# Kernel tuning notes

Hardware: AMD Instinct MI355X
Metric: run time of the kernel (lower is better)

The kernel has to match this reference:

```python
import jax, jax.numpy as jnp
import numpy as np

B, N_PTS, M_ROIS = 2, 8192, 2048
C_IN, O, H, NS = 128, 256, 4, 32
RADIUS = 1.6
BN_EPS = 1e-5
SCALE = 10.0  # point cloud extent


def setup_inputs() -> dict:
    key = jax.random.key(0)
    ks = jax.random.split(key, 20)
    f32 = jnp.float32
    Cg = C_IN + 3  # grouper concats relative xyz to features

    def kaiming(k, shape, fan_in):
        return jax.random.normal(k, shape, f32) * np.sqrt(2.0 / fan_in)

    inp = {
        "xyz": jax.random.uniform(ks[0], (B, N_PTS, 3), f32) * SCALE,
        "new_xyz": jax.random.uniform(ks[1], (B, M_ROIS, 3), f32) * SCALE,
        "features": jax.random.normal(ks[2], (B, C_IN, N_PTS), f32),
        # conv1d (kernel=1, no bias) weights, torch layout (out, in)
        "pos_w": kaiming(ks[3], (O, 3), 3),
        "key_w": kaiming(ks[4], (O, Cg), Cg),
        "val_w1": kaiming(ks[5], (O, Cg), Cg),
        "bn1_g": jnp.ones((O,), f32), "bn1_b": jnp.zeros((O,), f32),
        "val_w2": kaiming(ks[6], (O, O), O),
        "bn2_g": jnp.ones((O,), f32), "bn2_b": jnp.zeros((O,), f32),
        "attn_w": kaiming(ks[7], (H, O), O),
        # sigmoid-gated coefficient linears (no bias)
        "kc_w": kaiming(ks[8], (O, O), O),
        "qc_w": kaiming(ks[9], (O, O), O),
        "qkc_w": kaiming(ks[10], (O, O), O),
        "vc_w": kaiming(ks[11], (O, O), O),
        # cls/reg weight MLPs: Linear(O,O//2)+ReLU, Linear(O//2,1)+Sigmoid
        "cls_w1": kaiming(ks[12], (O // 2, O), O), "cls_b1": jnp.zeros((O // 2,), f32),
        "cls_w2": kaiming(ks[13], (1, O // 2), O // 2), "cls_b2": jnp.zeros((1,), f32),
        "reg_w1": kaiming(ks[14], (O // 2, O), O), "reg_b1": jnp.zeros((O // 2,), f32),
        "reg_w2": kaiming(ks[15], (1, O // 2), O // 2), "reg_b2": jnp.zeros((1,), f32),
    }
    return inp


def _bn(x, g, b):
    # eval-mode BatchNorm1d with running_mean=0, running_var=1 (init state)
    return g[None, :, None] * (x * (1.0 / np.sqrt(1.0 + BN_EPS))) + b[None, :, None]


def _conv1x1(w, x):  # (O,C) x (M,C,NS) -> (M,O,NS)
    return jnp.einsum('oc,mcn->mon', w, x)


def _ball_group(pts, q):
    # ball query: first NS points within RADIUS of each query (pad with first hit)
    n_tot = pts.shape[0]
    d2 = jnp.sum((q[:, None, :] - pts[None, :, :]) ** 2, axis=-1)  # (M, Ntot)
    order = jnp.where(d2 < RADIUS ** 2, jnp.arange(n_tot, dtype=jnp.int32), n_tot)
    neg_vals, idx = jax.lax.top_k(-order, NS)  # smallest indices among in-ball pts
    valid = (-neg_vals) < n_tot
    idx = jnp.where(valid, idx, idx[:, :1])  # pad with first neighbor
    has_any = valid[:, :1]
    idx = jnp.where(has_any, idx, 0)  # empty balls -> point 0
    return idx, ~has_any[:, 0]


def reference(xyz, new_xyz, features, pos_w, key_w, val_w1, bn1_g, bn1_b,
              val_w2, bn2_g, bn2_b, attn_w, kc_w, qc_w, qkc_w, vc_w,
              cls_w1, cls_b1, cls_w2, cls_b2, reg_w1, reg_b1, reg_w2, reg_b2):
    pts = xyz.reshape(-1, 3)                                   # (Ntot, 3)
    feats = features.transpose(0, 2, 1).reshape(-1, C_IN)      # (Ntot, C)
    q = new_xyz.reshape(-1, 3)                                 # (M, 3)

    idx, empty_mask = _ball_group(pts, q)                      # (M, NS)
    gx = pts[idx] - q[:, None, :]                              # relative xyz (M,NS,3)
    gxt = gx.transpose(0, 2, 1)                                # (M,3,NS)
    gf = jnp.concatenate([gx, feats[idx]], axis=-1).transpose(0, 2, 1)  # (M,C+3,NS)

    pos = jax.nn.relu(_conv1x1(pos_w, gxt))                    # (M,O,NS)
    key = jax.nn.relu(_conv1x1(key_w, gf))                     # (M,O,NS)
    v = jax.nn.relu(_bn(_conv1x1(val_w1, gf), bn1_g, bn1_b))
    val = jax.nn.relu(_bn(_conv1x1(val_w2, v), bn2_g, bn2_b))  # (M,O,NS)
    pos_key = pos * key

    sig = jax.nn.sigmoid
    v_c = sig(pos.mean(2) @ vc_w.T)                            # (M,O)
    q_c = sig(pos.mean(2) @ qc_w.T)
    k_c = sig(key.mean(2) @ kc_w.T)
    qk_c = sig(pos_key.mean(2) @ qkc_w.T)

    val = val + pos * v_c[:, :, None]
    attn_emb = pos * q_c[:, :, None] + key * k_c[:, :, None] + pos_key * qk_c[:, :, None]
    attn = jax.nn.softmax(jnp.einsum('ho,mon->mhn', attn_w, attn_emb), axis=-1)  # (M,H,NS)

    m = val.shape[0]
    vh = val.reshape(m, H, O // H, NS)
    new_features = jnp.einsum('mhdn,mhn->mhd', vh, attn).reshape(m, O)  # (M,O)

    def gate(x, w1, b1, w2, b2):
        return sig(jax.nn.relu(x @ w1.T + b1) @ w2.T + b2)

    cls_features = new_features * gate(new_features, cls_w1, cls_b1, cls_w2, cls_b2)
    reg_features = new_features * gate(new_features, reg_w1, reg_b1, reg_w2, reg_b2)
    return new_features, cls_features, reg_features
```

## Files before the change

kernel.cpp:

```cpp
#include <hip/hip_runtime.h>

#define DI __device__ __forceinline__

typedef __attribute__((ext_vector_type(8))) short bf16x8;
typedef __attribute__((ext_vector_type(4))) short s16x4;
typedef __attribute__((ext_vector_type(4))) float f32x4;

DI short f2bs(float x){ unsigned u = __float_as_uint(x);
  return (short)((u + 0x7FFF + ((u >> 16) & 1)) >> 16); }
DI float bs2f(short s){ return __uint_as_float(((unsigned)(unsigned short)s) << 16); }
DI f32x4 MFMA(bf16x8 a, bf16x8 b, f32x4 c){
  return __builtin_amdgcn_mfma_f32_16x16x32_bf16(a, b, c, 0, 0, 0);
}

constexpr int NP   = 8192;
constexpr int NTOT = 16384;
constexpr int M    = 4096;
constexpr int C    = 128;
constexpr int O    = 256;
constexpr int NS   = 32;
constexpr int H    = 4;
constexpr int KP   = 160;
constexpr int GFS  = 168;
constexpr int VS   = 264;
constexpr float BNS = 0.99999500003749969f;

DI void copy_rows(short* __restrict__ dst, const short* __restrict__ src, int t){
  int row = t >> 3, s = (t & 7) * 8;
  const short* sp = src + row*VS + s;
  short* dp = dst + (size_t)row*O + s;
  #pragma unroll
  for(int j = 0; j < 4; j++)
    *(bf16x8*)(dp + j*64) = *(const bf16x8*)(sp + j*64);
}

__global__ __launch_bounds__(256) void k_transpose(const float* __restrict__ feat,
                                                   short* __restrict__ fT){
  __shared__ float tile[128][65];
  int blk = blockIdx.x;
  int b  = blk >> 7;
  int n0 = (blk & 127) << 6;
  int t = threadIdx.x;
  int nn = t & 63, c4 = t >> 6;
  const float* src = feat + (size_t)b * C * NP;
  for(int i = 0; i < 32; i++){
    int c = c4 * 32 + i;
    tile[c][nn] = src[(size_t)c * NP + n0 + nn];
  }
  __syncthreads();
  int c2 = t & 127, nb = t >> 7;
  for(int j = 0; j < 32; j++){
    int n = nb + j * 2;
    fT[((size_t)(b * NP + n0 + n)) * C + c2] = f2bs(tile[c2][n]);
  }
}

__global__ __launch_bounds__(256) void k_pack(
    const float* __restrict__ kw, const float* __restrict__ v1w,
    const float* __restrict__ v2w,
    const float* __restrict__ vcw, const float* __restrict__ qcw,
    const float* __restrict__ kcw, const float* __restrict__ qkcw,
    const float* __restrict__ cw1, const float* __restrict__ rw1,
    short* __restrict__ keyP, short* __restrict__ v1P,
    short* __restrict__ v2b,
    short* __restrict__ gw,
    short* __restrict__ cw1b, short* __restrict__ rw1b)
{
  int i = blockIdx.x * 256 + threadIdx.x;
  if(i < O * KP){
    int o = i / KP, k = i % KP;
    float a = 0.0f, b = 0.0f;
    if(k < 128){ a = kw[o*131 + 3 + k]; b = v1w[o*131 + 3 + k]; }
    else if(k < 131){ a = kw[o*131 + (k - 128)]; b = v1w[o*131 + (k - 128)]; }
    keyP[i] = f2bs(a);
    v1P[i]  = f2bs(b);
  }
  if(i < O * O){
    v2b[i] = f2bs(v2w[i]);
    gw[0*O*O + i] = f2bs(vcw[i]);
    gw[1*O*O + i] = f2bs(qcw[i]);
    gw[2*O*O + i] = f2bs(kcw[i]);
    gw[3*O*O + i] = f2bs(qkcw[i]);
  }
  if(i < (O/2) * O){
    cw1b[i] = f2bs(cw1[i]);
    rw1b[i] = f2bs(rw1[i]);
  }
}

__global__ __launch_bounds__(64) void k_ballq(const float* __restrict__ xyz,
                                              const float* __restrict__ nxyz,
                                              int* __restrict__ idxo,
                                              float* __restrict__ gxo){
#pragma clang fp contract(off)
  int m = blockIdx.x;
  int lane = threadIdx.x;
  float qx = nxyz[m*3+0], qy = nxyz[m*3+1], qz = nxyz[m*3+2];
  __shared__ int sel[NS];
  int cnt = 0;
  for(int base = 0; base < NTOT; base += 64){
    int p = base + lane;
    float dx = qx - xyz[p*3+0], dy = qy - xyz[p*3+1], dz = qz - xyz[p*3+2];
    float d2 = dx*dx + dy*dy;
    d2 = d2 + dz*dz;
    bool pred = d2 < 2.56f;
    unsigned long long bal = __ballot(pred);
    if(pred){
      int pos = cnt + __popcll(bal & ((1ull << lane) - 1ull));
      if(pos < NS) sel[pos] = p;
    }
    cnt += __popcll(bal);
    if(cnt >= NS) break;
  }
  __syncthreads();
  if(lane < NS){
    int s = 0;
    if(cnt > 0) s = (lane < cnt) ? sel[lane] : sel[0];
    idxo[m*NS + lane] = s;
    gxo[(m*NS+lane)*3+0] = xyz[s*3+0] - qx;
    gxo[(m*NS+lane)*3+1] = xyz[s*3+1] - qy;
    gxo[(m*NS+lane)*3+2] = xyz[s*3+2] - qz;
  }
}

__global__ __launch_bounds__(256, 5) void k_conv(
    const short* __restrict__ fT,
    const short* __restrict__ keyP, const short* __restrict__ v1P,
    const short* __restrict__ v2b,
    const float* __restrict__ posw,
    const float* __restrict__ g1, const float* __restrict__ b1,
    const float* __restrict__ g2, const float* __restrict__ b2,
    const int* __restrict__ idxw, const float* __restrict__ gxw,
    short* __restrict__ keyo, short* __restrict__ valo,
    float* __restrict__ mPos, float* __restrict__ mKey, float* __restrict__ mPK,
    int q0)
{
  int lq = blockIdx.x, q = q0 + lq, t = threadIdx.x;
  int w = t >> 6, l = t & 63;
  int col = l & 15, kq = l >> 4;
  int ro = w * 64;
  __shared__ __align__(16) short gf[NS * GFS];
  __shared__ __align__(16) short vbuf[NS * VS];
  __shared__ float gxs[NS * 4];
  __shared__ int  sel[NS];
  if(t < NS){
    sel[t] = idxw[q*NS + t];
    gxs[t*4+0] = gxw[(q*NS+t)*3+0];
    gxs[t*4+1] = gxw[(q*NS+t)*3+1];
    gxs[t*4+2] = gxw[(q*NS+t)*3+2];
    gxs[t*4+3] = 0.0f;
  }
  __syncthreads();
  for(int i = 0; i < 8; i++){
    int n = w*8 + i;
    int p = sel[n];
    *(unsigned*)&gf[n*GFS + l*2] = *(const unsigned*)(fT + (size_t)p * C + l*2);
  }
  {
    int n = t & 31, kk = (t >> 5) * 4;
    for(int j = 0; j < 4; j++){
      int k = kk + j;
      float v = (k < 3) ? gxs[n*4 + k] : 0.0f;
      gf[n*GFS + 128 + k] = f2bs(v);
    }
  }
  __syncthreads();

  float posR[4][2][4];
  for(int mt=0;mt<4;mt++) for(int r=0;r<4;r++){
    int o = ro + mt*16 + kq*4 + r;
    float w0 = posw[o*3+0], w1 = posw[o*3+1], w2 = posw[o*3+2];
    for(int nt=0;nt<2;nt++){
      int n = nt*16 + col;
      posR[mt][nt][r] = fmaxf(w0*gxs[n*4+0] + w1*gxs[n*4+1] + w2*gxs[n*4+2], 0.0f);
    }
  }

  f32x4 acc[4][2];
  const f32x4 vzero = {0.0f, 0.0f, 0.0f, 0.0f};

  for(int mt=0;mt<4;mt++) for(int nt=0;nt<2;nt++) acc[mt][nt] = vzero;
  for(int ks = 0; ks < 5; ks++){
    bf16x8 b0 = *(const bf16x8*)&gf[col*GFS + ks*32 + kq*8];
    bf16x8 b1v = *(const bf16x8*)&gf[(16+col)*GFS + ks*32 + kq*8];
    for(int mt = 0; mt < 4; mt++){
      bf16x8 a = *(const bf16x8*)(keyP + (size_t)(ro + mt*16 + col)*KP + ks*32 + kq*8);
      acc[mt][0] = MFMA(a, b0, acc[mt][0]);
      acc[mt][1] = MFMA(a, b1v, acc[mt][1]);
    }
  }
  float mS[4][4][3];
  for(int mt=0;mt<4;mt++){
    for(int nt=0;nt<2;nt++){
      s16x4 pk;
      for(int r=0;r<4;r++){
        float v = fmaxf(acc[mt][nt][r], 0.0f);
        pk[r] = f2bs(v);
        if(nt == 0){ mS[mt][r][0] = posR[mt][0][r];  mS[mt][r][1] = v;
                     mS[mt][r][2] = posR[mt][0][r]*v; }
        else       { mS[mt][r][0] += posR[mt][1][r]; mS[mt][r][1] += v;
                     mS[mt][r][2] += posR[mt][1][r]*v; }
      }
      int n = nt*16 + col;
      *(s16x4*)&vbuf[n*VS + ro + mt*16 + kq*4] = pk;
    }
  }
  __syncthreads();
  copy_rows(keyo + (size_t)lq*NS*O, vbuf, t);
  for(int mt=0;mt<4;mt++) for(int r=0;r<4;r++){
    float sp = mS[mt][r][0], sk = mS[mt][r][1], spk = mS[mt][r][2];
    for(int msk=1; msk<16; msk<<=1){
      sp += __shfl_xor(sp, msk); sk += __shfl_xor(sk, msk); spk += __shfl_xor(spk, msk);
    }
    if(col == 0){
      int o = ro + mt*16 + kq*4 + r;
      mPos[lq*O+o] = sp  * 0.03125f;
      mKey[lq*O+o] = sk  * 0.03125f;
      mPK [lq*O+o] = spk * 0.03125f;
    }
  }

  for(int mt=0;mt<4;mt++) for(int nt=0;nt<2;nt++) acc[mt][nt] = vzero;
  for(int ks = 0; ks < 5; ks++){
    bf16x8 b0 = *(const bf16x8*)&gf[col*GFS + ks*32 + kq*8];
    bf16x8 b1v = *(const bf16x8*)&gf[(16+col)*GFS + ks*32 + kq*8];
    for(int mt = 0; mt < 4; mt++){
      bf16x8 a = *(const bf16x8*)(v1P + (size_t)(ro + mt*16 + col)*KP + ks*32 + kq*8);
      acc[mt][0] = MFMA(a, b0, acc[mt][0]);
      acc[mt][1] = MFMA(a, b1v, acc[mt][1]);
    }
  }
  __syncthreads();
  for(int mt=0;mt<4;mt++){
    int o0 = ro + mt*16 + kq*4;
    float gg[4], bb[4];
    for(int r=0;r<4;r++){ gg[r] = g1[o0+r]; bb[r] = b1[o0+r]; }
    for(int nt=0;nt<2;nt++){
      s16x4 pk;
      for(int r=0;r<4;r++)
        pk[r] = f2bs(fmaxf(gg[r]*(acc[mt][nt][r] * BNS) + bb[r], 0.0f));
      int n = nt*16 + col;
      *(s16x4*)&vbuf[n*VS + o0] = pk;
    }
  }
  __syncthreads();

  for(int mt=0;mt<4;mt++) for(int nt=0;nt<2;nt++) acc[mt][nt] = vzero;
  for(int ks = 0; ks < 8; ks++){
    bf16x8 b0 = *(const bf16x8*)&vbuf[col*VS + ks*32 + kq*8];
    bf16x8 b1v = *(const bf16x8*)&vbuf[(16+col)*VS + ks*32 + kq*8];
    for(int mt = 0; mt < 4; mt++){
      bf16x8 a = *(const bf16x8*)(v2b + (size_t)(ro + mt*16 + col)*O + ks*32 + kq*8);
      acc[mt][0] = MFMA(a, b0, acc[mt][0]);
      acc[mt][1] = MFMA(a, b1v, acc[mt][1]);
    }
  }
  s16x4 valS[4][2];
  for(int mt=0;mt<4;mt++){
    int o0 = ro + mt*16 + kq*4;
    float gg[4], bb[4];
    for(int r=0;r<4;r++){ gg[r] = g2[o0+r]; bb[r] = b2[o0+r]; }
    for(int nt=0;nt<2;nt++)
      for(int r=0;r<4;r++)
        valS[mt][nt][r] = f2bs(fmaxf(gg[r]*(acc[mt][nt][r] * BNS) + bb[r], 0.0f));
  }
  __syncthreads();
  for(int mt=0;mt<4;mt++) for(int nt=0;nt<2;nt++){
    int n = nt*16 + col;
    *(s16x4*)&vbuf[n*VS + ro + mt*16 + kq*4] = valS[mt][nt];
  }
  __syncthreads();
  copy_rows(valo + (size_t)lq*NS*O, vbuf, t);
}

__global__ __launch_bounds__(256) void k_gates(
    const float* __restrict__ mPos, const float* __restrict__ mKey,
    const float* __restrict__ mPK, const short* __restrict__ gw,
    float* __restrict__ gates)
{
  int t = threadIdx.x, w = t >> 6, l = t & 63, col = l & 15, kq = l >> 4;
  int lq0 = blockIdx.x * 16;
  const float* A  = (w < 2) ? mPos : ((w == 2) ? mKey : mPK);
  const short* Wg = gw + (size_t)w * O * O;
  f32x4 acc[16];
  const f32x4 vzero = {0.0f,0.0f,0.0f,0.0f};
  for(int i=0;i<16;i++) acc[i] = vzero;
  for(int ks = 0; ks < 8; ks++){
    union { bf16x8 v; short e[8]; } u;
    const float* ap = A + (size_t)(lq0 + col)*O + ks*32 + kq*8;
    for(int j = 0; j < 8; j++) u.e[j] = f2bs(ap[j]);
    for(int nt = 0; nt < 16; nt++){
      bf16x8 bv = *(const bf16x8*)(Wg + (size_t)(nt*16 + col)*O + ks*32 + kq*8);
      acc[nt] = MFMA(u.v, bv, acc[nt]);
    }
  }
  for(int nt=0;nt<16;nt++) for(int r=0;r<4;r++){
    int lqq = lq0 + kq*4 + r;
    int oo = nt*16 + col;
    gates[((size_t)lqq*4 + w)*O + oo] = 1.0f / (1.0f + expf(-acc[nt][r]));
  }
}

__global__ __launch_bounds__(256) void k_attn(
    const short* __restrict__ keyw, const short* __restrict__ valw,
    const float* __restrict__ gxw, const float* __restrict__ posw,
    const float* __restrict__ attw, const float* __restrict__ gates,
    float* __restrict__ outNF, int q0)
{
  int lq = blockIdx.x, q = q0 + lq, t = threadIdx.x;
  __shared__ float emL[O * 33];
  __shared__ float attnL[H * NS];
  __shared__ float gxs[NS * 3];
  __shared__ float partial[256];
  if(t < 96) gxs[t] = gxw[q*96 + t];
  float vc  = gates[((size_t)lq*4 + 0)*O + t];
  float qc  = gates[((size_t)lq*4 + 1)*O + t];
  float kc  = gates[((size_t)lq*4 + 2)*O + t];
  float qkc = gates[((size_t)lq*4 + 3)*O + t];
  float pw0 = posw[t*3+0], pw1 = posw[t*3+1], pw2 = posw[t*3+2];
  __syncthreads();
  float posr[NS];
  for(int n = 0; n < NS; n++)
    posr[n] = fmaxf(pw0*gxs[n*3] + pw1*gxs[n*3+1] + pw2*gxs[n*3+2], 0.0f);
  for(int n = 0; n < NS; n++){
    float k = bs2f(keyw[((size_t)lq*NS + n)*O + t]);
    emL[t*33 + n] = posr[n]*qc + k*kc + posr[n]*k*qkc;
  }
  __syncthreads();
  {
    int idx = t & 127, h = idx >> 5, n = idx & 31, half = t >> 7;
    float s = 0;
    const float* aw = attw + h*O + half*128;
    for(int o = 0; o < 128; o++) s += aw[o] * emL[(half*128 + o)*33 + n];
    partial[t] = s;
  }
  __syncthreads();
  if(t < 128){
    int h = t >> 5, n = t & 31;
    float s = partial[t] + partial[t + 128];
    float mx = s;
    for(int msk=1; msk<32; msk<<=1) mx = fmaxf(mx, __shfl_xor(mx, msk));
    float e = expf(s - mx);
    float sum = e;
    for(int msk=1; msk<32; msk<<=1) sum += __shfl_xor(sum, msk);
    attnL[h*NS + n] = e / sum;
  }
  __syncthreads();
  int h = t >> 6;
  float nf = 0;
  for(int n = 0; n < NS; n++){
    float v = bs2f(valw[((size_t)lq*NS + n)*O + t]);
    nf += (v + posr[n]*vc) * attnL[h*NS + n];
  }
  outNF[(size_t)q*O + t] = nf;
}

__global__ __launch_bounds__(256) void k_fgate(
    const float* __restrict__ nf,
    const short* __restrict__ cw1b, const float* __restrict__ cb1,
    const float* __restrict__ cw2, const float* __restrict__ cb2,
    const short* __restrict__ rw1b, const float* __restrict__ rb1,
    const float* __restrict__ rw2, const float* __restrict__ rb2,
    float* __restrict__ outC, float* __restrict__ outR)
{
  int t = threadIdx.x, w = t >> 6, l = t & 63, col = l & 15, kq = l >> 4;
  int q0 = blockIdx.x * 64;
  __shared__ float sC[64], sR[64];
  f32x4 acc[16];
  const f32x4 vzero = {0.0f,0.0f,0.0f,0.0f};
  for(int i=0;i<16;i++) acc[i] = vzero;
  int arow = q0 + w*16 + col;
  for(int ks = 0; ks < 8; ks++){
    union { bf16x8 v; short e[8]; } u;
    const float* ap = nf + (size_t)arow*O + ks*32 + kq*8;
    for(int j = 0; j < 8; j++) u.e[j] = f2bs(ap[j]);
    for(int nt = 0; nt < 16; nt++){
      const short* W1 = (nt < 8) ? cw1b : rw1b;
      int j = (nt & 7)*16 + col;
      bf16x8 bv = *(const bf16x8*)(W1 + (size_t)j*O + ks*32 + kq*8);
      acc[nt] = MFMA(u.v, bv, acc[nt]);
    }
  }
  for(int r = 0; r < 4; r++){
    float pc = 0, pr = 0;
    for(int nt = 0; nt < 8; nt++){
      int j = nt*16 + col;
      pc += fmaxf(acc[nt][r] + cb1[j], 0.0f) * cw2[j];
    }
    for(int nt = 8; nt < 16; nt++){
      int j = (nt - 8)*16 + col;
      pr += fmaxf(acc[nt][r] + rb1[j], 0.0f) * rw2[j];
    }
    for(int msk=1; msk<16; msk<<=1){ pc += __shfl_xor(pc, msk); pr += __shfl_xor(pr, msk); }
    if(col == 0){
      int qq = w*16 + kq*4 + r;
      sC[qq] = 1.0f / (1.0f + expf(-(pc + cb2[0])));
      sR[qq] = 1.0f / (1.0f + expf(-(pr + rb2[0])));
    }
  }
  __syncthreads();
  for(int qq = 0; qq < 64; qq++){
    float nv = nf[(size_t)(q0 + qq)*O + t];
    outC[(size_t)(q0 + qq)*O + t] = nv * sC[qq];
    outR[(size_t)(q0 + qq)*O + t] = nv * sR[qq];
  }
}

extern "C" void kernel_launch(void* const* d_in, const int* in_sizes, int n_in,
                              void* d_out, int out_size, void* d_ws, size_t ws_size,
                              hipStream_t stream)
{
  const float* xyz  = (const float*)d_in[0];
  const float* nxyz = (const float*)d_in[1];
  const float* feat = (const float*)d_in[2];
  const float* posw = (const float*)d_in[3];
  const float* keyw = (const float*)d_in[4];
  const float* v1w  = (const float*)d_in[5];
  const float* bn1g = (const float*)d_in[6];
  const float* bn1b = (const float*)d_in[7];
  const float* v2w  = (const float*)d_in[8];
  const float* bn2g = (const float*)d_in[9];
  const float* bn2b = (const float*)d_in[10];
  const float* attw = (const float*)d_in[11];
  const float* kcw  = (const float*)d_in[12];
  const float* qcw  = (const float*)d_in[13];
  const float* qkcw = (const float*)d_in[14];
  const float* vcw  = (const float*)d_in[15];
  const float* cw1  = (const float*)d_in[16];
  const float* cb1  = (const float*)d_in[17];
  const float* cw2  = (const float*)d_in[18];
  const float* cb2  = (const float*)d_in[19];
  const float* rw1  = (const float*)d_in[20];
  const float* rb1  = (const float*)d_in[21];
  const float* rw2  = (const float*)d_in[22];
  const float* rb2  = (const float*)d_in[23];

  const size_t fixedB = 12000000;
  const size_t perQ   = 40960;
  int Q = 64;
  for(int cand : {4096, 2048, 1024, 512, 256, 128}){
    if(fixedB + (size_t)cand*perQ <= ws_size){ Q = cand; break; }
  }

  char* p = (char*)d_ws;
  auto alloc = [&](size_t bytes){ char* r = p; p += (bytes + 255) & ~size_t(255); return r; };
  short* fT    = (short*)alloc((size_t)NTOT*C*2);
  short* keyP  = (short*)alloc((size_t)O*KP*2);
  short* v1P   = (short*)alloc((size_t)O*KP*2);
  short* v2b   = (short*)alloc((size_t)O*O*2);
  short* gw    = (short*)alloc((size_t)4*O*O*2);
  short* cw1b  = (short*)alloc((size_t)(O/2)*O*2);
  short* rw1b  = (short*)alloc((size_t)(O/2)*O*2);
  int*   idxw  = (int*)  alloc((size_t)M*NS*4);
  float* gxw   = (float*)alloc((size_t)M*NS*3*4);
  short* keyo  = (short*)alloc((size_t)Q*NS*O*2);
  short* valo  = (short*)alloc((size_t)Q*NS*O*2);
  float* mPos  = (float*)alloc((size_t)Q*O*4);
  float* mKey  = (float*)alloc((size_t)Q*O*4);
  float* mPK   = (float*)alloc((size_t)Q*O*4);
  float* gates = (float*)alloc((size_t)Q*4*O*4);

  float* outNF = (float*)d_out;
  float* outC  = outNF + (size_t)M*O;
  float* outR  = outC  + (size_t)M*O;

  k_transpose<<<256, 256, 0, stream>>>(feat, fT);
  k_pack     <<<256, 256, 0, stream>>>(keyw, v1w, v2w, vcw, qcw, kcw, qkcw, cw1, rw1,
                                       keyP, v1P, v2b, gw, cw1b, rw1b);
  k_ballq    <<<M,   64,  0, stream>>>(xyz, nxyz, idxw, gxw);
  for(int q0 = 0; q0 < M; q0 += Q){
    k_conv  <<<Q,    256, 0, stream>>>(fT, keyP, v1P, v2b,
                                       posw, bn1g, bn1b, bn2g, bn2b,
                                       idxw, gxw, keyo, valo, mPos, mKey, mPK, q0);
    k_gates <<<Q/16, 256, 0, stream>>>(mPos, mKey, mPK, gw, gates);
    k_attn  <<<Q,    256, 0, stream>>>(keyo, valo, gxw, posw, attw, gates, outNF, q0);
  }
  k_fgate   <<<M/64, 256, 0, stream>>>(outNF, cw1b, cb1, cw2, cb2, rw1b, rb1, rw2, rb2, outC, outR);
}
```

Baseline: 413.0 us.

## Recompute key conv to fuse attention into conv kernel, dropping key/val buffers

The conv kernel is split in two. A new k_means pass recomputes the key conv only to produce the pooled means, and a fused kernel recomputes key, value and pos, then applies the gates, softmax attention and the weighted sum entirely in registers and LDS. This removes the global write and re-read of the per-point key and value tensors (M×32×256 bf16 each) and drops the separate attention kernel. The cost is running the key GEMM and the gather twice, plus lower occupancy from the launch bound of 4 and extra LDS. The means are also stored as bf16, which halves that traffic but adds rounding.

```diff
diff --git a/kernel.cpp b/kernel.cpp
--- a/kernel.cpp
+++ b/kernel.cpp
@@ -24,15 +24,6 @@
 constexpr int GFS  = 168;
 constexpr int VS   = 264;
 constexpr float BNS = 0.99999500003749969f;
-
-DI void copy_rows(short* __restrict__ dst, const short* __restrict__ src, int t){
-  int row = t >> 3, s = (t & 7) * 8;
-  const short* sp = src + row*VS + s;
-  short* dp = dst + (size_t)row*O + s;
-  #pragma unroll
-  for(int j = 0; j < 4; j++)
-    *(bf16x8*)(dp + j*64) = *(const bf16x8*)(sp + j*64);
-}
 
 __global__ __launch_bounds__(256) void k_transpose(const float* __restrict__ feat,
                                                    short* __restrict__ fT){
@@ -123,17 +114,112 @@
   }
 }
 
-__global__ __launch_bounds__(256, 5) void k_conv(
+__global__ __launch_bounds__(256, 4) void k_means(
+    const short* __restrict__ fT, const short* __restrict__ keyP,
+    const float* __restrict__ posw,
+    const int* __restrict__ idxw, const float* __restrict__ gxw,
+    short* __restrict__ mPos, short* __restrict__ mKey, short* __restrict__ mPK,
+    int q0)
+{
+  int lq = blockIdx.x, q = q0 + lq, t = threadIdx.x;
+  int w = t >> 6, l = t & 63;
+  int col = l & 15, kq = l >> 4;
+  int ro = w * 64;
+  __shared__ __align__(16) short gf[NS * GFS];
+  __shared__ float gxs[NS * 4];
+  __shared__ int  sel[NS];
+  if(t < NS){
+    sel[t] = idxw[q*NS + t];
+    gxs[t*4+0] = gxw[(q*NS+t)*3+0];
+    gxs[t*4+1] = gxw[(q*NS+t)*3+1];
+    gxs[t*4+2] = gxw[(q*NS+t)*3+2];
+    gxs[t*4+3] = 0.0f;
+  }
+  __syncthreads();
+  for(int i = 0; i < 8; i++){
+    int n = w*8 + i;
+    int p = sel[n];
+    *(unsigned*)&gf[n*GFS + l*2] = *(const unsigned*)(fT + (size_t)p * C + l*2);
+  }
+  {
+    int n = t & 31, kk = (t >> 5) * 4;
+    for(int j = 0; j < 4; j++){
+      int k = kk + j;
+      float v = (k < 3) ? gxs[n*4 + k] : 0.0f;
+      gf[n*GFS + 128 + k] = f2bs(v);
+    }
+  }
+  __syncthreads();
+
+  f32x4 acc[4][2];
+  const f32x4 vzero = {0.0f, 0.0f, 0.0f, 0.0f};
+  for(int mt=0;mt<4;mt++) for(int nt=0;nt<2;nt++) acc[mt][nt] = vzero;
+  for(int ks = 0; ks < 5; ks++){
+    bf16x8 b0 = *(const bf16x8*)&gf[col*GFS + ks*32 + kq*8];
+    bf16x8 b1v = *(const bf16x8*)&gf[(16+col)*GFS + ks*32 + kq*8];
+    for(int mt = 0; mt < 4; mt++){
+      bf16x8 a = *(const bf16x8*)(keyP + (size_t)(ro + mt*16 + col)*KP + ks*32 + kq*8);
+      acc[mt][0] = MFMA(a, b0, acc[mt][0]);
+      acc[mt][1] = MFMA(a, b1v, acc[mt][1]);
+    }
+  }
+  for(int mt=0;mt<4;mt++) for(int r=0;r<4;r++){
+    int o = ro + mt*16 + kq*4 + r;
+    float w0 = posw[o*3+0], w1 = posw[o*3+1], w2 = posw[o*3+2];
+    float sp = 0, sk = 0, spk = 0;
+    for(int nt=0;nt<2;nt++){
+      int n = nt*16 + col;
+      float p = fmaxf(w0*gxs[n*4+0] + w1*gxs[n*4+1] + w2*gxs[n*4+2], 0.0f);
+      float v = fmaxf(acc[mt][nt][r], 0.0f);
+      sp += p; sk += v; spk += p*v;
+    }
+    for(int msk=1; msk<16; msk<<=1){
+      sp += __shfl_xor(sp, msk); sk += __shfl_xor(sk, msk); spk += __shfl_xor(spk, msk);
+    }
+    if(col == 0){
+      mPos[lq*O+o] = f2bs(sp  * 0.03125f);
+      mKey[lq*O+o] = f2bs(sk  * 0.03125f);
+      mPK [lq*O+o] = f2bs(spk * 0.03125f);
+    }
+  }
+}
+
+__global__ __launch_bounds__(256) void k_gates(
+    const short* __restrict__ mPos, const short* __restrict__ mKey,
+    const short* __restrict__ mPK, const short* __restrict__ gw,
+    float* __restrict__ gates)
+{
+  int t = threadIdx.x, w = t >> 6, l = t & 63, col = l & 15, kq = l >> 4;
+  int lq0 = blockIdx.x * 16;
+  const short* A  = (w < 2) ? mPos : ((w == 2) ? mKey : mPK);
+  const short* Wg = gw + (size_t)w * O * O;
+  f32x4 acc[16];
+  const f32x4 vzero = {0.0f,0.0f,0.0f,0.0f};
+  for(int i=0;i<16;i++) acc[i] = vzero;
+  for(int ks = 0; ks < 8; ks++){
+    bf16x8 av = *(const bf16x8*)(A + (size_t)(lq0 + col)*O + ks*32 + kq*8);
+    for(int nt = 0; nt < 16; nt++){
+      bf16x8 bv = *(const bf16x8*)(Wg + (size_t)(nt*16 + col)*O + ks*32 + kq*8);
+      acc[nt] = MFMA(av, bv, acc[nt]);
+    }
+  }
+  for(int nt=0;nt<16;nt++) for(int r=0;r<4;r++){
+    int lqq = lq0 + kq*4 + r;
+    int oo = nt*16 + col;
+    gates[((size_t)lqq*4 + w)*O + oo] = 1.0f / (1.0f + expf(-acc[nt][r]));
+  }
+}
+
+__global__ __launch_bounds__(256, 4) void k_fused(
     const short* __restrict__ fT,
     const short* __restrict__ keyP, const short* __restrict__ v1P,
     const short* __restrict__ v2b,
     const float* __restrict__ posw,
     const float* __restrict__ g1, const float* __restrict__ b1,
     const float* __restrict__ g2, const float* __restrict__ b2,
+    const float* __restrict__ attw, const float* __restrict__ gates,
     const int* __restrict__ idxw, const float* __restrict__ gxw,
-    short* __restrict__ keyo, short* __restrict__ valo,
-    float* __restrict__ mPos, float* __restrict__ mKey, float* __restrict__ mPK,
-    int q0)
+    float* __restrict__ outNF, int q0)
 {
   int lq = blockIdx.x, q = q0 + lq, t = threadIdx.x;
   int w = t >> 6, l = t & 63;
@@ -143,12 +229,18 @@
   __shared__ __align__(16) short vbuf[NS * VS];
   __shared__ float gxs[NS * 4];
   __shared__ int  sel[NS];
+  __shared__ float gatesL[4 * O];
+  __shared__ float attwL[4 * O];
   if(t < NS){
     sel[t] = idxw[q*NS + t];
     gxs[t*4+0] = gxw[(q*NS+t)*3+0];
     gxs[t*4+1] = gxw[(q*NS+t)*3+1];
     gxs[t*4+2] = gxw[(q*NS+t)*3+2];
     gxs[t*4+3] = 0.0f;
+  }
+  for(int g = 0; g < 4; g++){
+    gatesL[g*O + t] = gates[((size_t)lq*4 + g)*O + t];
+    attwL [g*O + t] = attw[g*O + t];
   }
   __syncthreads();
   for(int i = 0; i < 8; i++){
@@ -189,36 +281,10 @@
       acc[mt][1] = MFMA(a, b1v, acc[mt][1]);
     }
   }
-  float mS[4][4][3];
-  for(int mt=0;mt<4;mt++){
-    for(int nt=0;nt<2;nt++){
-      s16x4 pk;
-      for(int r=0;r<4;r++){
-        float v = fmaxf(acc[mt][nt][r], 0.0f);
-        pk[r] = f2bs(v);
-        if(nt == 0){ mS[mt][r][0] = posR[mt][0][r];  mS[mt][r][1] = v;
-                     mS[mt][r][2] = posR[mt][0][r]*v; }
-        else       { mS[mt][r][0] += posR[mt][1][r]; mS[mt][r][1] += v;
-                     mS[mt][r][2] += posR[mt][1][r]*v; }
-      }
-      int n = nt*16 + col;
-      *(s16x4*)&vbuf[n*VS + ro + mt*16 + kq*4] = pk;
-    }
-  }
-  __syncthreads();
-  copy_rows(keyo + (size_t)lq*NS*O, vbuf, t);
-  for(int mt=0;mt<4;mt++) for(int r=0;r<4;r++){
-    float sp = mS[mt][r][0], sk = mS[mt][r][1], spk = mS[mt][r][2];
-    for(int msk=1; msk<16; msk<<=1){
-      sp += __shfl_xor(sp, msk); sk += __shfl_xor(sk, msk); spk += __shfl_xor(spk, msk);
-    }
-    if(col == 0){
-      int o = ro + mt*16 + kq*4 + r;
-      mPos[lq*O+o] = sp  * 0.03125f;
-      mKey[lq*O+o] = sk  * 0.03125f;
-      mPK [lq*O+o] = spk * 0.03125f;
-    }
-  }
+  s16x4 keyB[4][2];
+  for(int mt=0;mt<4;mt++) for(int nt=0;nt<2;nt++)
+    for(int r=0;r<4;r++)
+      keyB[mt][nt][r] = f2bs(fmaxf(acc[mt][nt][r], 0.0f));
 
   for(int mt=0;mt<4;mt++) for(int nt=0;nt<2;nt++) acc[mt][nt] = vzero;
   for(int ks = 0; ks < 5; ks++){
@@ -231,6 +297,10 @@
     }
   }
   __syncthreads();
+
+  float* sPart = reinterpret_cast<float*>(gf);
+  float* attnL = reinterpret_cast<float*>(gf) + 512;
+
   for(int mt=0;mt<4;mt++){
     int o0 = ro + mt*16 + kq*4;
     float gg[4], bb[4];
@@ -243,6 +313,35 @@
       *(s16x4*)&vbuf[n*VS + o0] = pk;
     }
   }
+
+  {
+    float sh0[2] = {0,0}, sh1[2] = {0,0}, sh2[2] = {0,0}, sh3[2] = {0,0};
+    for(int mt=0;mt<4;mt++) for(int r=0;r<4;r++){
+      int o = ro + mt*16 + kq*4 + r;
+      float qc = gatesL[1*O+o], kc = gatesL[2*O+o], qkc = gatesL[3*O+o];
+      float a0 = attwL[0*O+o], a1 = attwL[1*O+o], a2 = attwL[2*O+o], a3 = attwL[3*O+o];
+      for(int nt=0;nt<2;nt++){
+        float p = posR[mt][nt][r];
+        float k = bs2f(keyB[mt][nt][r]);
+        float e = p*qc + k*kc + p*k*qkc;
+        sh0[nt] += a0*e; sh1[nt] += a1*e; sh2[nt] += a2*e; sh3[nt] += a3*e;
+      }
+    }
+    for(int nt=0;nt<2;nt++){
+      float v0 = sh0[nt], v1 = sh1[nt], v2 = sh2[nt], v3 = sh3[nt];
+      v0 += __shfl_xor(v0,16); v0 += __shfl_xor(v0,32);
+      v1 += __shfl_xor(v1,16); v1 += __shfl_xor(v1,32);
+      v2 += __shfl_xor(v2,16); v2 += __shfl_xor(v2,32);
+      v3 += __shfl_xor(v3,16); v3 += __shfl_xor(v3,32);
+      if(kq == 0){
+        int n = nt*16 + col;
+        sPart[(w*4+0)*32 + n] = v0;
+        sPart[(w*4+1)*32 + n] = v1;
+        sPart[(w*4+2)*32 + n] = v2;
+        sPart[(w*4+3)*32 + n] = v3;
+      }
+    }
+  }
   __syncthreads();
 
   for(int mt=0;mt<4;mt++) for(int nt=0;nt<2;nt++) acc[mt][nt] = vzero;
@@ -255,89 +354,20 @@
       acc[mt][1] = MFMA(a, b1v, acc[mt][1]);
     }
   }
-  s16x4 valS[4][2];
+  float valR[4][2][4];
   for(int mt=0;mt<4;mt++){
     int o0 = ro + mt*16 + kq*4;
     float gg[4], bb[4];
     for(int r=0;r<4;r++){ gg[r] = g2[o0+r]; bb[r] = b2[o0+r]; }
     for(int nt=0;nt<2;nt++)
       for(int r=0;r<4;r++)
-        valS[mt][nt][r] = f2bs(fmaxf(gg[r]*(acc[mt][nt][r] * BNS) + bb[r], 0.0f));
-  }
-  __syncthreads();
-  for(int mt=0;mt<4;mt++) for(int nt=0;nt<2;nt++){
-    int n = nt*16 + col;
-    *(s16x4*)&vbuf[n*VS + ro + mt*16 + kq*4] = valS[mt][nt];
-  }
-  __syncthreads();
-  copy_rows(valo + (size_t)lq*NS*O, vbuf, t);
-}
-
-__global__ __launch_bounds__(256) void k_gates(
-    const float* __restrict__ mPos, const float* __restrict__ mKey,
-    const float* __restrict__ mPK, const short* __restrict__ gw,
-    float* __restrict__ gates)
-{
-  int t = threadIdx.x, w = t >> 6, l = t & 63, col = l & 15, kq = l >> 4;
-  int lq0 = blockIdx.x * 16;
-  const float* A  = (w < 2) ? mPos : ((w == 2) ? mKey : mPK);
-  const short* Wg = gw + (size_t)w * O * O;
-  f32x4 acc[16];
-  const f32x4 vzero = {0.0f,0.0f,0.0f,0.0f};
-  for(int i=0;i<16;i++) acc[i] = vzero;
-  for(int ks = 0; ks < 8; ks++){
-    union { bf16x8 v; short e[8]; } u;
-    const float* ap = A + (size_t)(lq0 + col)*O + ks*32 + kq*8;
-    for(int j = 0; j < 8; j++) u.e[j] = f2bs(ap[j]);
-    for(int nt = 0; nt < 16; nt++){
-      bf16x8 bv = *(const bf16x8*)(Wg + (size_t)(nt*16 + col)*O + ks*32 + kq*8);
-      acc[nt] = MFMA(u.v, bv, acc[nt]);
-    }
-  }
-  for(int nt=0;nt<16;nt++) for(int r=0;r<4;r++){
-    int lqq = lq0 + kq*4 + r;
-    int oo = nt*16 + col;
-    gates[((size_t)lqq*4 + w)*O + oo] = 1.0f / (1.0f + expf(-acc[nt][r]));
-  }
-}
-
-__global__ __launch_bounds__(256) void k_attn(
-    const short* __restrict__ keyw, const short* __restrict__ valw,
-    const float* __restrict__ gxw, const float* __restrict__ posw,
-    const float* __restrict__ attw, const float* __restrict__ gates,
-    float* __restrict__ outNF, int q0)
-{
-  int lq = blockIdx.x, q = q0 + lq, t = threadIdx.x;
-  __shared__ float emL[O * 33];
-  __shared__ float attnL[H * NS];
-  __shared__ float gxs[NS * 3];
-  __shared__ float partial[256];
-  if(t < 96) gxs[t] = gxw[q*96 + t];
-  float vc  = gates[((size_t)lq*4 + 0)*O + t];
-  float qc  = gates[((size_t)lq*4 + 1)*O + t];
-  float kc  = gates[((size_t)lq*4 + 2)*O + t];
-  float qkc = gates[((size_t)lq*4 + 3)*O + t];
-  float pw0 = posw[t*3+0], pw1 = posw[t*3+1], pw2 = posw[t*3+2];
-  __syncthreads();
-  float posr[NS];
-  for(int n = 0; n < NS; n++)
-    posr[n] = fmaxf(pw0*gxs[n*3] + pw1*gxs[n*3+1] + pw2*gxs[n*3+2], 0.0f);
-  for(int n = 0; n < NS; n++){
-    float k = bs2f(keyw[((size_t)lq*NS + n)*O + t]);
-    emL[t*33 + n] = posr[n]*qc + k*kc + posr[n]*k*qkc;
-  }
-  __syncthreads();
-  {
-    int idx = t & 127, h = idx >> 5, n = idx & 31, half = t >> 7;
-    float s = 0;
-    const float* aw = attw + h*O + half*128;
-    for(int o = 0; o < 128; o++) s += aw[o] * emL[(half*128 + o)*33 + n];
-    partial[t] = s;
-  }
-  __syncthreads();
+        valR[mt][nt][r] = fmaxf(gg[r]*(acc[mt][nt][r] * BNS) + bb[r], 0.0f);
+  }
+
   if(t < 128){
     int h = t >> 5, n = t & 31;
-    float s = partial[t] + partial[t + 128];
+    float s = sPart[(0*4+h)*32 + n] + sPart[(1*4+h)*32 + n]
+            + sPart[(2*4+h)*32 + n] + sPart[(3*4+h)*32 + n];
     float mx = s;
     for(int msk=1; msk<32; msk<<=1) mx = fmaxf(mx, __shfl_xor(mx, msk));
     float e = expf(s - mx);
@@ -346,13 +376,19 @@
     attnL[h*NS + n] = e / sum;
   }
   __syncthreads();
-  int h = t >> 6;
-  float nf = 0;
-  for(int n = 0; n < NS; n++){
-    float v = bs2f(valw[((size_t)lq*NS + n)*O + t]);
-    nf += (v + posr[n]*vc) * attnL[h*NS + n];
-  }
-  outNF[(size_t)q*O + t] = nf;
+
+  {
+    float a0 = attnL[w*NS + col];
+    float a1 = attnL[w*NS + 16 + col];
+    for(int mt=0;mt<4;mt++) for(int r=0;r<4;r++){
+      int o = ro + mt*16 + kq*4 + r;
+      float vc = gatesL[0*O + o];
+      float nf = (valR[mt][0][r] + posR[mt][0][r]*vc) * a0
+               + (valR[mt][1][r] + posR[mt][1][r]*vc) * a1;
+      for(int msk=1; msk<16; msk<<=1) nf += __shfl_xor(nf, msk);
+      if(col == 0) outNF[(size_t)q*O + o] = nf;
+    }
+  }
 }
 
 __global__ __launch_bounds__(256) void k_fgate(
@@ -435,8 +471,8 @@
   const float* rw2  = (const float*)d_in[22];
   const float* rb2  = (const float*)d_in[23];
 
-  const size_t fixedB = 12000000;
-  const size_t perQ   = 40960;
+  const size_t fixedB = 7500000;
+  const size_t perQ   = 6144;
   int Q = 64;
   for(int cand : {4096, 2048, 1024, 512, 256, 128}){
     if(fixedB + (size_t)cand*perQ <= ws_size){ Q = cand; break; }
@@ -453,11 +489,9 @@
   short* rw1b  = (short*)alloc((size_t)(O/2)*O*2);
   int*   idxw  = (int*)  alloc((size_t)M*NS*4);
   float* gxw   = (float*)alloc((size_t)M*NS*3*4);
-  short* keyo  = (short*)alloc((size_t)Q*NS*O*2);
-  short* valo  = (short*)alloc((size_t)Q*NS*O*2);
-  float* mPos  = (float*)alloc((size_t)Q*O*4);
-  float* mKey  = (float*)alloc((size_t)Q*O*4);
-  float* mPK   = (float*)alloc((size_t)Q*O*4);
+  short* mPos  = (short*)alloc((size_t)Q*O*2);
+  short* mKey  = (short*)alloc((size_t)Q*O*2);
+  short* mPK   = (short*)alloc((size_t)Q*O*2);
   float* gates = (float*)alloc((size_t)Q*4*O*4);
 
   float* outNF = (float*)d_out;
@@ -469,11 +503,11 @@
                                        keyP, v1P, v2b, gw, cw1b, rw1b);
   k_ballq    <<<M,   64,  0, stream>>>(xyz, nxyz, idxw, gxw);
   for(int q0 = 0; q0 < M; q0 += Q){
-    k_conv  <<<Q,    256, 0, stream>>>(fT, keyP, v1P, v2b,
+    k_means <<<Q,    256, 0, stream>>>(fT, keyP, posw, idxw, gxw, mPos, mKey, mPK, q0);
+    k_gates <<<Q/16, 256, 0, stream>>>(mPos, mKey, mPK, gw, gates);
+    k_fused <<<Q,    256, 0, stream>>>(fT, keyP, v1P, v2b,
                                        posw, bn1g, bn1b, bn2g, bn2b,
-                                       idxw, gxw, keyo, valo, mPos, mKey, mPK, q0);
-    k_gates <<<Q/16, 256, 0, stream>>>(mPos, mKey, mPK, gw, gates);
-    k_attn  <<<Q,    256, 0, stream>>>(keyo, valo, gxw, posw, attw, gates, outNF, q0);
+                                       attw, gates, idxw, gxw, outNF, q0);
   }
   k_fgate   <<<M/64, 256, 0, stream>>>(outNF, cw1b, cb1, cw2, cb2, rw1b, rb1, rw2, rb2, outC, outR);
 }
```

New measurement: 480.7 us. 1.16x slower.

## Restructure attention kernel to drop large LDS buffer and use shuffle reductions

Applied to the files above, without the earlier changes.

Rewrites k_attn so each wave owns a 64-channel slice. Each thread computes the attention embedding for a few channels and points on the fly, accumulating per-head partial logits in registers and reducing them with cross-lane shuffles, instead of staging the full O×NS embedding in a 33 KB LDS buffer. Gates, attention weights and position weights are now cached in LDS, and the per-thread posr[32] register array is gone, with position features recomputed where needed. This is meant to raise occupancy and cut LDS traffic. The cost is recomputing position features, more shuffle reductions in the output stage, and global loads that are strided across points rather than contiguous.

```diff
diff --git a/kernel.cpp b/kernel.cpp
--- a/kernel.cpp
+++ b/kernel.cpp
@@ -308,36 +308,72 @@
     float* __restrict__ outNF, int q0)
 {
   int lq = blockIdx.x, q = q0 + lq, t = threadIdx.x;
-  __shared__ float emL[O * 33];
+  int w = t >> 6, l = t & 63;
+  int col = l & 15, kq = l >> 4;
+  int ro = w * 64;
+  __shared__ float gxs[NS * 4];
+  __shared__ float gatesL[4 * O];
+  __shared__ float attwL[4 * O];
+  __shared__ float posL[3 * O];
+  __shared__ float sPart[4 * 4 * NS];
   __shared__ float attnL[H * NS];
-  __shared__ float gxs[NS * 3];
-  __shared__ float partial[256];
-  if(t < 96) gxs[t] = gxw[q*96 + t];
-  float vc  = gates[((size_t)lq*4 + 0)*O + t];
-  float qc  = gates[((size_t)lq*4 + 1)*O + t];
-  float kc  = gates[((size_t)lq*4 + 2)*O + t];
-  float qkc = gates[((size_t)lq*4 + 3)*O + t];
-  float pw0 = posw[t*3+0], pw1 = posw[t*3+1], pw2 = posw[t*3+2];
-  __syncthreads();
-  float posr[NS];
-  for(int n = 0; n < NS; n++)
-    posr[n] = fmaxf(pw0*gxs[n*3] + pw1*gxs[n*3+1] + pw2*gxs[n*3+2], 0.0f);
-  for(int n = 0; n < NS; n++){
-    float k = bs2f(keyw[((size_t)lq*NS + n)*O + t]);
-    emL[t*33 + n] = posr[n]*qc + k*kc + posr[n]*k*qkc;
-  }
-  __syncthreads();
-  {
-    int idx = t & 127, h = idx >> 5, n = idx & 31, half = t >> 7;
-    float s = 0;
-    const float* aw = attw + h*O + half*128;
-    for(int o = 0; o < 128; o++) s += aw[o] * emL[(half*128 + o)*33 + n];
-    partial[t] = s;
-  }
-  __syncthreads();
+  if(t < NS){
+    gxs[t*4+0] = gxw[(q*NS+t)*3+0];
+    gxs[t*4+1] = gxw[(q*NS+t)*3+1];
+    gxs[t*4+2] = gxw[(q*NS+t)*3+2];
+    gxs[t*4+3] = 0.0f;
+  }
+  for(int g = 0; g < 4; g++){
+    gatesL[g*O + t] = gates[((size_t)lq*4 + g)*O + t];
+    attwL [g*O + t] = attw[g*O + t];
+  }
+  for(int j = 0; j < 3; j++) posL[j*256 + t] = posw[j*256 + t];
+  __syncthreads();
+
+  const short* keyQ = keyw + (size_t)lq*NS*O;
+  float shp[4][2];
+  #pragma unroll
+  for(int h=0;h<4;h++){ shp[h][0] = 0.0f; shp[h][1] = 0.0f; }
+  #pragma unroll
+  for(int mt=0;mt<4;mt++){
+    #pragma unroll
+    for(int nt=0;nt<2;nt++){
+      int n = nt*16 + col;
+      s16x4 kf = *(const s16x4*)(keyQ + (size_t)n*O + ro + mt*16 + kq*4);
+      #pragma unroll
+      for(int r=0;r<4;r++){
+        int o = ro + mt*16 + kq*4 + r;
+        float w0 = posL[o*3+0], w1 = posL[o*3+1], w2 = posL[o*3+2];
+        float p = fmaxf(w0*gxs[n*4+0] + w1*gxs[n*4+1] + w2*gxs[n*4+2], 0.0f);
+        float k = bs2f(kf[r]);
+        float qc = gatesL[1*O+o], kc = gatesL[2*O+o], qkc = gatesL[3*O+o];
+        float e = p*qc + k*kc + p*k*qkc;
+        shp[0][nt] += attwL[0*O+o]*e; shp[1][nt] += attwL[1*O+o]*e;
+        shp[2][nt] += attwL[2*O+o]*e; shp[3][nt] += attwL[3*O+o]*e;
+      }
+    }
+  }
+  #pragma unroll
+  for(int nt=0;nt<2;nt++){
+    float v0 = shp[0][nt], v1 = shp[1][nt], v2 = shp[2][nt], v3 = shp[3][nt];
+    v0 += __shfl_xor(v0,16); v0 += __shfl_xor(v0,32);
+    v1 += __shfl_xor(v1,16); v1 += __shfl_xor(v1,32);
+    v2 += __shfl_xor(v2,16); v2 += __shfl_xor(v2,32);
+    v3 += __shfl_xor(v3,16); v3 += __shfl_xor(v3,32);
+    if(kq == 0){
+      int n = nt*16 + col;
+      sPart[(w*4+0)*NS + n] = v0;
+      sPart[(w*4+1)*NS + n] = v1;
+      sPart[(w*4+2)*NS + n] = v2;
+      sPart[(w*4+3)*NS + n] = v3;
+    }
+  }
+  __syncthreads();
+
   if(t < 128){
     int h = t >> 5, n = t & 31;
-    float s = partial[t] + partial[t + 128];
+    float s = sPart[(0*4+h)*NS + n] + sPart[(1*4+h)*NS + n]
+            + sPart[(2*4+h)*NS + n] + sPart[(3*4+h)*NS + n];
     float mx = s;
     for(int msk=1; msk<32; msk<<=1) mx = fmaxf(mx, __shfl_xor(mx, msk));
     float e = expf(s - mx);
@@ -346,13 +382,27 @@
     attnL[h*NS + n] = e / sum;
   }
   __syncthreads();
-  int h = t >> 6;
-  float nf = 0;
-  for(int n = 0; n < NS; n++){
-    float v = bs2f(valw[((size_t)lq*NS + n)*O + t]);
-    nf += (v + posr[n]*vc) * attnL[h*NS + n];
-  }
-  outNF[(size_t)q*O + t] = nf;
+
+  const short* valQ = valw + (size_t)lq*NS*O;
+  float a0 = attnL[w*NS + col];
+  float a1 = attnL[w*NS + 16 + col];
+  #pragma unroll
+  for(int mt=0;mt<4;mt++){
+    s16x4 vf0 = *(const s16x4*)(valQ + (size_t)col*O      + ro + mt*16 + kq*4);
+    s16x4 vf1 = *(const s16x4*)(valQ + (size_t)(16+col)*O + ro + mt*16 + kq*4);
+    #pragma unroll
+    for(int r=0;r<4;r++){
+      int o = ro + mt*16 + kq*4 + r;
+      float w0 = posL[o*3+0], w1 = posL[o*3+1], w2 = posL[o*3+2];
+      float vc = gatesL[0*O + o];
+      int n0 = col, n1 = 16 + col;
+      float p0 = fmaxf(w0*gxs[n0*4+0] + w1*gxs[n0*4+1] + w2*gxs[n0*4+2], 0.0f);
+      float p1 = fmaxf(w0*gxs[n1*4+0] + w1*gxs[n1*4+1] + w2*gxs[n1*4+2], 0.0f);
+      float nf = (bs2f(vf0[r]) + p0*vc) * a0 + (bs2f(vf1[r]) + p1*vc) * a1;
+      for(int msk=1; msk<16; msk<<=1) nf += __shfl_xor(nf, msk);
+      if(col == 0) outNF[(size_t)q*O + o] = nf;
+    }
+  }
 }
 
 __global__ __launch_bounds__(256) void k_fgate(
```

Result: slower. 441.0 us (+6.8%).
